# Performance work log

Hardware: AMD Instinct MI355X
Metric: run time of the kernel (lower is better)

## Reference

```python
import jax, jax.numpy as jnp
import numpy as np
from jax import lax

B, T, E, H, ENC, NUM_LAYERS = 256, 100, 300, 512, 1024, 3
FORGET_BIAS = 1.0  # BasicLSTMCell default


def lstm_scan(x, W, b):
    """BasicLSTMCell over time. x: [B,T,E], W: [E+H,4H], b: [4H] -> hs: [B,T,H]."""
    def step(carry, xt):
        c, h = carry
        z = jnp.concatenate([xt, h], axis=-1) @ W + b  # [B,4H]
        i, j, f, o = jnp.split(z, 4, axis=-1)  # TF gate order i, j, f, o
        c = c * jax.nn.sigmoid(f + FORGET_BIAS) + jax.nn.sigmoid(i) * jnp.tanh(j)
        h = jnp.tanh(c) * jax.nn.sigmoid(o)
        return (c, h), h
    init = (jnp.zeros((x.shape[0], W.shape[1] // 4), x.dtype),) * 2
    _, hs = lax.scan(step, init, jnp.swapaxes(x, 0, 1))  # scan over T
    return jnp.swapaxes(hs, 0, 1)  # [B,T,H]


def last_output(hs, lengths):
    # reverse_sequence + slice[:, 0, :] == output at step length-1
    return hs[jnp.arange(hs.shape[0]), lengths - 1]  # [B,H]


def setup_inputs() -> dict:
    key = jax.random.key(0)
    ks = jax.random.split(key, 10)
    scale = 0.01  # random_normal_initializer(stddev=1/100)
    return {
        "left_embed": jax.random.normal(ks[0], (B, T, E), jnp.float32),
        "left_lengths": jax.random.randint(ks[1], (B,), 1, T + 1, jnp.int32),
        "right_embed": jax.random.normal(ks[2], (B, T, E), jnp.float32),
        "right_lengths": jax.random.randint(ks[3], (B,), 1, T + 1, jnp.int32),
        "W_left": jax.random.normal(ks[4], (E + H, 4 * H), jnp.float32) / np.sqrt(E + H),
        "b_left": jnp.zeros((4 * H,), jnp.float32),
        "W_right": jax.random.normal(ks[5], (E + H, 4 * H), jnp.float32) / np.sqrt(E + H),
        "b_right": jnp.zeros((4 * H,), jnp.float32),
        "trans_weights": scale * jax.random.normal(ks[6], (2 * H, ENC), jnp.float32),
        "hidden_weights": scale * jax.random.normal(ks[7], (NUM_LAYERS - 1, ENC, ENC), jnp.float32),
    }


def reference(left_embed, left_lengths, right_embed, right_lengths,
              W_left, b_left, W_right, b_right, trans_weights, hidden_weights):
    l_last = last_output(lstm_scan(left_embed, W_left, b_left), left_lengths)
    r_last = last_output(lstm_scan(right_embed, W_right, b_right), right_lengths)
    ctx = jnp.concatenate([l_last, r_last], axis=1)  # [B, 2H]
    x = jax.nn.relu(ctx @ trans_weights)
    for i in range(hidden_weights.shape[0]):  # dropout keep_prob=1.0 -> identity
        x = jax.nn.relu(x @ hidden_weights[i])
    return x  # [B, ENC]
```

## Files before the change

### kernel.cpp

```cpp
#include <hip/hip_runtime.h>
#include <math.h>

#define EDIM 300
#define HDIM 512
#define TDIM 100
#define BDIM 256
#define ENC  1024
#define NBLK 256

#define B_C     0u
#define B_HPK   1048576u
#define B_WXF   3145728u
#define B_WHF   5767168u
#define B_CTX   9961472u
#define B_X1    11010048u
#define B_X2    12058624u
#define B_TWH   13107200u
#define B_TWL   19398656u
#define B_ZX    25690112u

typedef __attribute__((ext_vector_type(8))) short bf16x8;
typedef _Float16 f16x8 __attribute__((ext_vector_type(8)));
typedef __attribute__((ext_vector_type(4))) float f32x4;
typedef __attribute__((ext_vector_type(4))) unsigned int u32x4;

__device__ __forceinline__ float fast_sigmoid(float x) {
    return 1.0f / (1.0f + __expf(-x));
}
__device__ __forceinline__ float fast_tanh(float x) {
    float t = __expf(2.0f * x);
    return 1.0f - 2.0f / (t + 1.0f);
}
__device__ __forceinline__ unsigned short bf16_rne(float v) {
    unsigned int u = __float_as_uint(v);
    unsigned int r = (u + 0x7fffu + ((u >> 16) & 1u)) >> 16;
    return (unsigned short)r;
}
__device__ __forceinline__ float bf16_to_f(unsigned short h) {
    return __uint_as_float(((unsigned int)h) << 16);
}
__device__ __forceinline__ void split2(float v, unsigned short& hi, unsigned short& lo) {
    hi = bf16_rne(v);
    lo = bf16_rne(v - bf16_to_f(hi));
}
__device__ __forceinline__ unsigned short f16_bits(float v) {
    _Float16 h = (_Float16)v;
    return *(unsigned short*)&h;
}
__device__ __forceinline__ float f16_val(unsigned short u) {
    _Float16 h = *(_Float16*)&u;
    return (float)h;
}
__device__ __forceinline__ void split_f16(float v, unsigned short& hi, unsigned short& lo) {
    hi = f16_bits(v);
    lo = f16_bits(v - f16_val(hi));
}

__global__ void zero_kernel(float* __restrict__ p, int n) {
    int i = blockIdx.x * blockDim.x + threadIdx.x;
    if (i < n) p[i] = 0.0f;
}

__global__ __launch_bounds__(256) void prep_wx(
    const float* __restrict__ WL, const float* __restrict__ WR, char* __restrict__ ws)
{
    __shared__ float tile[64 * 65];
    int bid = blockIdx.x;
    int d = bid / (5 * 32);
    int rem = bid - d * (5 * 32);
    int kt = rem >> 5;
    int ct = rem & 31;
    const int k0 = kt * 64;
    const float* W = d ? WR : WL;
    for (int pass = 0; pass < 16; ++pass) {
        int idx = pass * 256 + threadIdx.x;
        int kk = idx >> 6, c = idx & 63;
        int g = (c >> 4) & 3, hl = c & 15;
        int col = g * HDIM + ct * 16 + hl;
        int kg = k0 + kk;
        tile[kk * 65 + c] = (kg < EDIM) ? W[(size_t)kg * 2048 + col] : 0.0f;
    }
    __syncthreads();
    unsigned short* wx = (unsigned short*)(ws + B_WXF) + (size_t)d * 2048 * 320;
    for (int pass = 0; pass < 16; ++pass) {
        int idx = pass * 256 + threadIdx.x;
        int c = idx >> 6, kk = idx & 63;
        wx[(size_t)(ct * 64 + c) * 320 + k0 + kk] = f16_bits(tile[kk * 65 + c]);
    }
}

__global__ __launch_bounds__(256) void prep_whf(
    const float* __restrict__ WL, const float* __restrict__ WR, char* __restrict__ ws)
{
    __shared__ float tile[64 * 65];
    int bid = blockIdx.x;
    int d = bid >> 8;
    int rem = bid & 255;
    int kt = rem >> 5;
    int ct = rem & 31;
    const float* W = d ? WR : WL;
    for (int pass = 0; pass < 16; ++pass) {
        int idx = pass * 256 + threadIdx.x;
        int kk = idx >> 6, c = idx & 63;
        int g = (c >> 4) & 3, hl = c & 15;
        int col = g * HDIM + ct * 16 + hl;
        tile[kk * 65 + c] = W[(size_t)(300 + kt * 64 + kk) * 2048 + col];
    }
    __syncthreads();
    unsigned short* dst = (unsigned short*)(ws + B_WHF) + ((size_t)(d * 32 + ct) * 64) * 512;
    #pragma unroll
    for (int p = 0; p < 2; ++p) {
        int item = p * 256 + threadIdx.x;
        int fl = item >> 6;
        int ls = item & 63;
        int itl = fl >> 2, nfl = fl & 3;
        int frag = (kt >> 2) * 32 + ((kt & 3) * 2 + itl) * 4 + nfl;
        __align__(16) unsigned short v[8];
        #pragma unroll
        for (int j = 0; j < 8; ++j)
            v[j] = f16_bits(tile[(itl * 32 + (ls >> 4) * 8 + j) * 65 + nfl * 16 + (ls & 15)]);
        *(uint4*)(dst + (size_t)frag * 512 + ls * 8) = *(uint4*)v;
    }
}

__global__ __launch_bounds__(256) void prep_w_tail(
    const float* __restrict__ TW, const float* __restrict__ HW, char* __restrict__ ws)
{
    __shared__ float tile[64 * 65];
    int bid = blockIdx.x;
    int l = bid / 256;
    int rem = bid - l * 256;
    int kt = rem >> 4, ct = rem & 15;
    const int k0 = kt * 64, n0 = ct * 64;
    const float* W = (l == 0) ? TW : (HW + (size_t)(l - 1) * ENC * ENC);
    for (int pass = 0; pass < 16; ++pass) {
        int idx = pass * 256 + threadIdx.x;
        int kk = idx >> 6, c = idx & 63;
        tile[kk * 65 + c] = W[(size_t)(k0 + kk) * ENC + n0 + c];
    }
    __syncthreads();
    unsigned short* wh = (unsigned short*)(ws + B_TWH) + (size_t)l * ENC * ENC;
    unsigned short* wl = (unsigned short*)(ws + B_TWL) + (size_t)l * ENC * ENC;
    for (int pass = 0; pass < 16; ++pass) {
        int idx = pass * 256 + threadIdx.x;
        int c = idx >> 6, kk = idx & 63;
        unsigned short hi, lo;
        split2(tile[kk * 65 + c], hi, lo);
        size_t o = (size_t)(n0 + c) * ENC + k0 + kk;
        wh[o] = hi;
        wl[o] = lo;
    }
}

__global__ __launch_bounds__(512, 4) void prep_zx(
    const float* __restrict__ xL, const float* __restrict__ xR,
    const float* __restrict__ bL, const float* __restrict__ bR,
    char* __restrict__ ws)
{
    __shared__ __align__(16) char smem[81920];
    const int ntile = blockIdx.x;
    const int m0    = blockIdx.y * 64;
    const int d     = blockIdx.z;
    const int n0    = ntile * 128;
    const float* __restrict__ x    = d ? xR : xL;
    const float* __restrict__ bias = d ? bR : bL;
    const unsigned short* __restrict__ Wxp = (const unsigned short*)(ws + B_WXF) + (size_t)d * 2048 * 320;
    unsigned short* __restrict__ zxd = (unsigned short*)(ws + B_ZX) + (size_t)d * TDIM * BDIM * 2048;

    const int tid = threadIdx.x;
    const int l   = tid & 63;
    const int w   = tid >> 6;
    const int kh  = w >> 2;
    const int ms  = w & 3;
    const int fr  = l & 15;
    const int fg  = l >> 4;

    #pragma unroll
    for (int j = 0; j < 10; ++j) {
        int c = j * 512 + tid;
        int frag = c >> 6, ls = c & 63;
        int khf = (frag >= 40) ? 1 : 0;
        int f2 = frag - khf * 40;
        int itf = f2 >> 3, nff = f2 & 7;
        int colp = n0 + nff * 16 + (ls & 15);
        int kk = khf * 160 + itf * 32 + (ls >> 4) * 8;
        *(uint4*)(smem + frag * 1024 + ls * 16) =
            *(const uint4*)(Wxp + (size_t)colp * 320 + kk);
    }
    __syncthreads();

    f32x4 acc[8] = {};
    const int rowX = m0 + ms * 16 + fr;
    const float* __restrict__ xrow = x + (size_t)rowX * EDIM;
    const int kb = kh * 160 + fg * 8;

    #pragma unroll
    for (int it = 0; it < 5; ++it) {
        const int kg = kb + it * 32;
        float4 f4a = (kg + 4 <= EDIM) ? *(const float4*)(xrow + kg) : make_float4(0.f, 0.f, 0.f, 0.f);
        float4 f4b = (kg + 8 <= EDIM) ? *(const float4*)(xrow + kg + 4) : make_float4(0.f, 0.f, 0.f, 0.f);
        __align__(16) unsigned short ahu[8], alu[8];
        float vv[8] = { f4a.x, f4a.y, f4a.z, f4a.w, f4b.x, f4b.y, f4b.z, f4b.w };
        #pragma unroll
        for (int i = 0; i < 8; ++i) {
            unsigned short hi, lo;
            split_f16(vv[i], hi, lo);
            ahu[i] = hi;
            alu[i] = lo;
        }
        const f16x8 ah = *(f16x8*)ahu;
        const f16x8 al = *(f16x8*)alu;
        #pragma unroll
        for (int nf = 0; nf < 8; ++nf) {
            const f16x8 bv = *(const f16x8*)(smem + ((kh * 40 + it * 8 + nf) << 10) + l * 16);
            acc[nf] = __builtin_amdgcn_mfma_f32_16x16x32_f16(ah, bv, acc[nf], 0, 0, 0);
            acc[nf] = __builtin_amdgcn_mfma_f32_16x16x32_f16(al, bv, acc[nf], 0, 0, 0);
        }
    }

    __syncthreads();
    float* red = (float*)smem;
    unsigned short* outT = (unsigned short*)(smem + 49152);
    if (kh == 1) {
        #pragma unroll
        for (int nf = 0; nf < 8; ++nf)
            #pragma unroll
            for (int r = 0; r < 4; ++r)
                red[(ms * 16 + fg * 4 + r) * 132 + nf * 16 + fr] = acc[nf][r];
    }
    __syncthreads();
    if (kh == 0) {
        #pragma unroll
        for (int nf = 0; nf < 8; ++nf) {
            const int col = (nf & 3) * HDIM + (ntile * 2 + (nf >> 2)) * 16 + fr;
            const float bv = bias[col];
            #pragma unroll
            for (int r = 0; r < 4; ++r) {
                float v = acc[nf][r] + red[(ms * 16 + fg * 4 + r) * 132 + nf * 16 + fr] + bv;
                outT[(ms * 16 + fg * 4 + r) * 128 + nf * 16 + fr] = f16_bits(v);
            }
        }
    }
    __syncthreads();
    {
        int row = tid >> 3, seg = tid & 7;
        int rm = m0 + row;
        int b = rm / 100;
        int tt = rm - b * 100;
        unsigned short* dstrow = zxd + ((size_t)(tt * 256 + b)) * 2048 + n0 + seg * 16;
        const unsigned short* s = outT + row * 128 + seg * 16;
        __builtin_nontemporal_store(*(const u32x4*)(s),     (u32x4*)(dstrow));
        __builtin_nontemporal_store(*(const u32x4*)(s + 8), (u32x4*)(dstrow + 8));
    }
}

__global__ __launch_bounds__(512, 1) void lstm_step_h(
    const int* __restrict__ lenL, const int* __restrict__ lenR,
    char* __restrict__ ws, int t, int par)
{
    __shared__ __align__(16) char smem[65536];

    const int bid   = blockIdx.x;
    const int ntile = (bid & 7) * 4 + ((bid >> 3) & 3);
    const int mt    = bid >> 5;
    const int n0    = ntile * 64;
    const int d     = mt >> 2;
    const int brow  = (mt & 3) * 64;

    const int* __restrict__ len = d ? lenR : lenL;

    float* __restrict__ cbuf = (float*)(ws + B_C);
    const unsigned short* __restrict__ hpk_prev = (const unsigned short*)(ws + B_HPK) + (size_t)par * 524288;
    unsigned short* __restrict__ hpk_next = (unsigned short*)(ws + B_HPK) + (size_t)(par ^ 1) * 524288;
    const unsigned short* __restrict__ WhF = (const unsigned short*)(ws + B_WHF);
    const unsigned short* __restrict__ zxd = (const unsigned short*)(ws + B_ZX) + (size_t)d * TDIM * BDIM * 2048;
    float* __restrict__ ctx = (float*)(ws + B_CTX);

    const int tid = threadIdx.x;
    const int l   = tid & 63;
    const int w   = tid >> 6;
    const int kh  = w >> 2;
    const int ms  = w & 3;
    const int fr  = l & 15;
    const int fg  = l >> 4;

    {
        const unsigned short* __restrict__ wsrc = WhF + ((size_t)(d * 32 + ntile) * 64) * 512;
        #pragma unroll
        for (int j = 0; j < 8; ++j) {
            const unsigned short* g = wsrc + (size_t)(j * 512 + tid) * 8;
            char* ldst = smem + ((size_t)(j * 512 + (w << 6)) * 16);
            __builtin_amdgcn_global_load_lds(
                (const __attribute__((address_space(1))) void*)(const void*)g,
                (__attribute__((address_space(3))) void*)(void*)ldst, 16, 0, 0);
        }
    }

    const int arow = d * BDIM + brow + ms * 16 + fr;
    const unsigned short* __restrict__ abase = hpk_prev + (size_t)arow * 1024;
    uint4 aph[8], apl[8];
    #pragma unroll
    for (int it = 0; it < 8; ++it) {
        const int kb = kh * 32 + it * 4 + fg;
        aph[it] = *(const uint4*)(abase + kb * 16);
        apl[it] = *(const uint4*)(abase + kb * 16 + 8);
    }

    const int hcol = ntile * 16 + fr;
    const int row0 = brow + ms * 16 + fg * 4;
    const int4 len4 = *(const int4*)(len + row0);
    float c_arr[4];
    unsigned short zraw[16];
    if (kh == 0) {
        const size_t cb = (size_t)(d * BDIM + row0) * HDIM + hcol;
        c_arr[0] = cbuf[cb];
        c_arr[1] = cbuf[cb + HDIM];
        c_arr[2] = cbuf[cb + 2 * HDIM];
        c_arr[3] = cbuf[cb + 3 * HDIM];
        const unsigned short* zb = zxd + ((size_t)(t * 256 + row0)) * 2048 + n0 + fr;
        #pragma unroll
        for (int r = 0; r < 4; ++r)
            #pragma unroll
            for (int nf = 0; nf < 4; ++nf)
                zraw[r * 4 + nf] = zb[r * 2048 + nf * 16];
    }
    __syncthreads();

    f32x4 acc[4] = {};
    #pragma unroll
    for (int it = 0; it < 8; ++it) {
        const f16x8 ah = *(const f16x8*)&aph[it];
        const f16x8 al = *(const f16x8*)&apl[it];
        #pragma unroll
        for (int nf = 0; nf < 4; ++nf) {
            const f16x8 bv = *(const f16x8*)(smem + ((kh * 32 + it * 4 + nf) << 10) + l * 16);
            acc[nf] = __builtin_amdgcn_mfma_f32_16x16x32_f16(ah, bv, acc[nf], 0, 0, 0);
            acc[nf] = __builtin_amdgcn_mfma_f32_16x16x32_f16(al, bv, acc[nf], 0, 0, 0);
        }
    }

    __syncthreads();
    float* red = (float*)smem;
    if (kh == 1) {
        #pragma unroll
        for (int nf = 0; nf < 4; ++nf)
            #pragma unroll
            for (int r = 0; r < 4; ++r)
                red[(ms * 16 + fg * 4 + r) * 65 + nf * 16 + fr] = acc[nf][r];
    }
    __syncthreads();
    if (kh == 0) {
        const int lens[4] = { len4.x, len4.y, len4.z, len4.w };
        #pragma unroll
        for (int r = 0; r < 4; ++r) {
            const int row = row0 + r;
            const int rb = (ms * 16 + fg * 4 + r) * 65;
            const float iv = acc[0][r] + red[rb + 0 * 16 + fr] + f16_val(zraw[r * 4 + 0]);
            const float jv = acc[1][r] + red[rb + 1 * 16 + fr] + f16_val(zraw[r * 4 + 1]);
            const float fv = acc[2][r] + red[rb + 2 * 16 + fr] + f16_val(zraw[r * 4 + 2]);
            const float ov = acc[3][r] + red[rb + 3 * 16 + fr] + f16_val(zraw[r * 4 + 3]);
            const float c_new = c_arr[r] * fast_sigmoid(fv + 1.0f)
                              + fast_sigmoid(iv) * fast_tanh(jv);
            const float h_new = fast_tanh(c_new) * fast_sigmoid(ov);
            const size_t cidx = (size_t)(d * BDIM + row) * HDIM + hcol;
            cbuf[cidx] = c_new;
            unsigned short hh, hl2;
            split_f16(h_new, hh, hl2);
            const size_t hidx = (size_t)(d * BDIM + row) * 1024 + (hcol >> 3) * 16 + (hcol & 7);
            hpk_next[hidx] = hh;
            hpk_next[hidx + 8] = hl2;
            if (t == lens[r] - 1) {
                ctx[(size_t)row * (2 * HDIM) + d * HDIM + hcol] = h_new;
            }
        }
    }
}

#define TL_AS_HI(hf) ((hf) * 5120)
#define TL_AS_LO(hf) (10240 + (hf) * 5120)
#define TL_BS_HI(hf) (20480 + (hf) * 5120)
#define TL_BS_LO(hf) (30720 + (hf) * 5120)

__global__ __launch_bounds__(512, 2) void gemm_relu_mfma(
    const float* __restrict__ A, const unsigned short* __restrict__ Wh,
    const unsigned short* __restrict__ Wl, float* __restrict__ C)
{
    const int ntile = blockIdx.x & 15;
    const int mt    = blockIdx.x >> 4;
    const int n0    = ntile * 64;
    const int m0    = mt * 64;

    __shared__ __align__(16) char smem[40960];

    const int tid  = threadIdx.x;
    const int l    = tid & 63;
    const int w    = tid >> 6;
    const int kh   = w >> 2;
    const int ms   = w & 3;
    const int fr   = l & 15;
    const int fg   = l >> 4;
    const int arow = tid >> 3;
    const int q    = (tid & 7) * 4;

    f32x4 acc[4] = {};

    for (int it = 0; it < 16; ++it) {
        #pragma unroll
        for (int hf = 0; hf < 2; ++hf) {
            const int kg = hf * 512 + it * 32 + q;
            const float4 v = *(const float4*)(A + (size_t)(m0 + arow) * ENC + kg);
            ushort4 vh, vl;
            split2(v.x, vh.x, vl.x);
            split2(v.y, vh.y, vl.y);
            split2(v.z, vh.z, vl.z);
            split2(v.w, vh.w, vl.w);
            *(ushort4*)(smem + TL_AS_HI(hf) + (arow * 40 + q) * 2) = vh;
            *(ushort4*)(smem + TL_AS_LO(hf) + (arow * 40 + q) * 2) = vl;
            const size_t wo = (size_t)(n0 + arow) * ENC + kg;
            *(ushort4*)(smem + TL_BS_HI(hf) + (arow * 40 + q) * 2) = *(const ushort4*)(Wh + wo);
            *(ushort4*)(smem + TL_BS_LO(hf) + (arow * 40 + q) * 2) = *(const ushort4*)(Wl + wo);
        }
        __syncthreads();
        const int aoff = ((ms * 16 + fr) * 40 + fg * 8) * 2;
        const bf16x8 ah = *(const bf16x8*)(smem + TL_AS_HI(kh) + aoff);
        const bf16x8 al = *(const bf16x8*)(smem + TL_AS_LO(kh) + aoff);
        #pragma unroll
        for (int nf = 0; nf < 4; ++nf) {
            const int boff = ((nf * 16 + fr) * 40 + fg * 8) * 2;
            const bf16x8 bh = *(const bf16x8*)(smem + TL_BS_HI(kh) + boff);
            const bf16x8 bl = *(const bf16x8*)(smem + TL_BS_LO(kh) + boff);
            acc[nf] = __builtin_amdgcn_mfma_f32_16x16x32_bf16(ah, bh, acc[nf], 0, 0, 0);
            acc[nf] = __builtin_amdgcn_mfma_f32_16x16x32_bf16(ah, bl, acc[nf], 0, 0, 0);
            acc[nf] = __builtin_amdgcn_mfma_f32_16x16x32_bf16(al, bh, acc[nf], 0, 0, 0);
        }
        __syncthreads();
    }

    float* red = (float*)smem;
    if (kh == 1) {
        #pragma unroll
        for (int nf = 0; nf < 4; ++nf)
            #pragma unroll
            for (int r = 0; r < 4; ++r)
                red[(ms * 16 + fg * 4 + r) * 65 + nf * 16 + fr] = acc[nf][r];
    }
    __syncthreads();
    if (kh == 0) {
        #pragma unroll
        for (int nf = 0; nf < 4; ++nf) {
            #pragma unroll
            for (int r = 0; r < 4; ++r) {
                float v = acc[nf][r] + red[(ms * 16 + fg * 4 + r) * 65 + nf * 16 + fr];
                v = v > 0.f ? v : 0.f;
                const int row = m0 + ms * 16 + fg * 4 + r;
                C[(size_t)row * ENC + n0 + nf * 16 + fr] = v;
            }
        }
    }
}

extern "C" void kernel_launch(void* const* d_in, const int* in_sizes, int n_in,
                              void* d_out, int out_size, void* d_ws, size_t ws_size,
                              hipStream_t stream) {
    const float* xL   = (const float*)d_in[0];
    const int*   lenL = (const int*)  d_in[1];
    const float* xR   = (const float*)d_in[2];
    const int*   lenR = (const int*)  d_in[3];
    const float* WL   = (const float*)d_in[4];
    const float* bL   = (const float*)d_in[5];
    const float* WR   = (const float*)d_in[6];
    const float* bR   = (const float*)d_in[7];
    const float* TW   = (const float*)d_in[8];
    const float* HW   = (const float*)d_in[9];
    char* ws   = (char*)d_ws;
    float* out = (float*)d_out;

    zero_kernel<<<3072, 256, 0, stream>>>((float*)ws, 786432);
    prep_wx<<<320, 256, 0, stream>>>(WL, WR, ws);
    prep_whf<<<512, 256, 0, stream>>>(WL, WR, ws);
    prep_w_tail<<<768, 256, 0, stream>>>(TW, HW, ws);
    prep_zx<<<dim3(16, 400, 2), 512, 0, stream>>>(xL, xR, bL, bR, ws);

    for (int t = 0; t < TDIM; ++t) {
        lstm_step_h<<<NBLK, 512, 0, stream>>>(lenL, lenR, ws, t, t & 1);
    }

    float* ctx = (float*)(ws + B_CTX);
    float* x1  = (float*)(ws + B_X1);
    float* x2  = (float*)(ws + B_X2);
    const unsigned short* twh = (const unsigned short*)(ws + B_TWH);
    const unsigned short* twl = (const unsigned short*)(ws + B_TWL);
    gemm_relu_mfma<<<64, 512, 0, stream>>>(ctx, twh,                twl,                x1);
    gemm_relu_mfma<<<64, 512, 0, stream>>>(x1,  twh + 1024 * 1024, twl + 1024 * 1024,  x2);
    gemm_relu_mfma<<<64, 512, 0, stream>>>(x2,  twh + 2048 * 1024, twl + 2048 * 1024,  out);
}
```

Measured before the change: 1.306 ms.

## Make prep_zx persistent over row tiles and split warps by N instead of K

The input-projection kernel now launches 16 row groups instead of 400, and each block loops over 25 row tiles of 64 rows. The staged weight tile is therefore loaded into shared memory once and reused across many tiles. Warps now partition the output columns rather than the K dimension, which removes the cross-warp shared-memory reduction and the extra barriers. The trade-off is that results are written straight to global memory as scattered 2-byte stores instead of coalesced 16-byte nontemporal stores, and the grid has far fewer blocks.

```diff
diff --git a/kernel.cpp b/kernel.cpp
--- a/kernel.cpp
+++ b/kernel.cpp
@@ -22,7 +22,6 @@
 typedef __attribute__((ext_vector_type(8))) short bf16x8;
 typedef _Float16 f16x8 __attribute__((ext_vector_type(8)));
 typedef __attribute__((ext_vector_type(4))) float f32x4;
-typedef __attribute__((ext_vector_type(4))) unsigned int u32x4;
 
 __device__ __forceinline__ float fast_sigmoid(float x) {
     return 1.0f / (1.0f + __expf(-x));
@@ -159,7 +158,7 @@
 {
     __shared__ __align__(16) char smem[81920];
     const int ntile = blockIdx.x;
-    const int m0    = blockIdx.y * 64;
+    const int mg    = blockIdx.y;
     const int d     = blockIdx.z;
     const int n0    = ntile * 128;
     const float* __restrict__ x    = d ? xR : xL;
@@ -170,7 +169,7 @@
     const int tid = threadIdx.x;
     const int l   = tid & 63;
     const int w   = tid >> 6;
-    const int kh  = w >> 2;
+    const int nh  = w >> 2;
     const int ms  = w & 3;
     const int fr  = l & 15;
     const int fg  = l >> 4;
@@ -179,78 +178,58 @@
     for (int j = 0; j < 10; ++j) {
         int c = j * 512 + tid;
         int frag = c >> 6, ls = c & 63;
-        int khf = (frag >= 40) ? 1 : 0;
-        int f2 = frag - khf * 40;
-        int itf = f2 >> 3, nff = f2 & 7;
-        int colp = n0 + nff * 16 + (ls & 15);
-        int kk = khf * 160 + itf * 32 + (ls >> 4) * 8;
+        int nfg = frag / 10, itf = frag - nfg * 10;
+        int colp = n0 + nfg * 16 + (ls & 15);
+        int kk = itf * 32 + (ls >> 4) * 8;
         *(uint4*)(smem + frag * 1024 + ls * 16) =
             *(const uint4*)(Wxp + (size_t)colp * 320 + kk);
     }
     __syncthreads();
 
-    f32x4 acc[8] = {};
-    const int rowX = m0 + ms * 16 + fr;
-    const float* __restrict__ xrow = x + (size_t)rowX * EDIM;
-    const int kb = kh * 160 + fg * 8;
-
-    #pragma unroll
-    for (int it = 0; it < 5; ++it) {
-        const int kg = kb + it * 32;
-        float4 f4a = (kg + 4 <= EDIM) ? *(const float4*)(xrow + kg) : make_float4(0.f, 0.f, 0.f, 0.f);
-        float4 f4b = (kg + 8 <= EDIM) ? *(const float4*)(xrow + kg + 4) : make_float4(0.f, 0.f, 0.f, 0.f);
-        __align__(16) unsigned short ahu[8], alu[8];
-        float vv[8] = { f4a.x, f4a.y, f4a.z, f4a.w, f4b.x, f4b.y, f4b.z, f4b.w };
-        #pragma unroll
-        for (int i = 0; i < 8; ++i) {
-            unsigned short hi, lo;
-            split_f16(vv[i], hi, lo);
-            ahu[i] = hi;
-            alu[i] = lo;
-        }
-        const f16x8 ah = *(f16x8*)ahu;
-        const f16x8 al = *(f16x8*)alu;
-        #pragma unroll
-        for (int nf = 0; nf < 8; ++nf) {
-            const f16x8 bv = *(const f16x8*)(smem + ((kh * 40 + it * 8 + nf) << 10) + l * 16);
-            acc[nf] = __builtin_amdgcn_mfma_f32_16x16x32_f16(ah, bv, acc[nf], 0, 0, 0);
-            acc[nf] = __builtin_amdgcn_mfma_f32_16x16x32_f16(al, bv, acc[nf], 0, 0, 0);
-        }
-    }
-
-    __syncthreads();
-    float* red = (float*)smem;
-    unsigned short* outT = (unsigned short*)(smem + 49152);
-    if (kh == 1) {
-        #pragma unroll
-        for (int nf = 0; nf < 8; ++nf)
-            #pragma unroll
-            for (int r = 0; r < 4; ++r)
-                red[(ms * 16 + fg * 4 + r) * 132 + nf * 16 + fr] = acc[nf][r];
-    }
-    __syncthreads();
-    if (kh == 0) {
-        #pragma unroll
-        for (int nf = 0; nf < 8; ++nf) {
-            const int col = (nf & 3) * HDIM + (ntile * 2 + (nf >> 2)) * 16 + fr;
-            const float bv = bias[col];
+    for (int mi = 0; mi < 25; ++mi) {
+        const int m0 = (mg * 25 + mi) * 64;
+        const int rowX = m0 + ms * 16 + fr;
+        const float* __restrict__ xrow = x + (size_t)rowX * EDIM;
+
+        f32x4 acc[4] = {};
+        #pragma unroll
+        for (int it = 0; it < 10; ++it) {
+            const int kg = it * 32 + fg * 8;
+            float4 f4a = (kg + 4 <= EDIM) ? *(const float4*)(xrow + kg) : make_float4(0.f, 0.f, 0.f, 0.f);
+            float4 f4b = (kg + 8 <= EDIM) ? *(const float4*)(xrow + kg + 4) : make_float4(0.f, 0.f, 0.f, 0.f);
+            __align__(16) unsigned short ahu[8], alu[8];
+            float vv[8] = { f4a.x, f4a.y, f4a.z, f4a.w, f4b.x, f4b.y, f4b.z, f4b.w };
+            #pragma unroll
+            for (int i = 0; i < 8; ++i) {
+                unsigned short hi, lo;
+                split_f16(vv[i], hi, lo);
+                ahu[i] = hi;
+                alu[i] = lo;
+            }
+            const f16x8 ah = *(f16x8*)ahu;
+            const f16x8 al = *(f16x8*)alu;
+            #pragma unroll
+            for (int nf = 0; nf < 4; ++nf) {
+                const int frag = (nh * 4 + nf) * 10 + it;
+                const f16x8 bv = *(const f16x8*)(smem + (frag << 10) + l * 16);
+                acc[nf] = __builtin_amdgcn_mfma_f32_16x16x32_f16(ah, bv, acc[nf], 0, 0, 0);
+                acc[nf] = __builtin_amdgcn_mfma_f32_16x16x32_f16(al, bv, acc[nf], 0, 0, 0);
+            }
+        }
+
+        #pragma unroll
+        for (int nf = 0; nf < 4; ++nf) {
+            const int colp = n0 + nh * 64 + nf * 16 + fr;
+            const int G = colp >> 6, g = (colp >> 4) & 3, hl = colp & 15;
+            const float bv = bias[g * HDIM + G * 16 + hl];
             #pragma unroll
             for (int r = 0; r < 4; ++r) {
-                float v = acc[nf][r] + red[(ms * 16 + fg * 4 + r) * 132 + nf * 16 + fr] + bv;
-                outT[(ms * 16 + fg * 4 + r) * 128 + nf * 16 + fr] = f16_bits(v);
+                const int rm = m0 + ms * 16 + fg * 4 + r;
+                const int b = rm / 100;
+                const int tt = rm - b * 100;
+                zxd[((size_t)(tt * 256 + b)) * 2048 + colp] = f16_bits(acc[nf][r] + bv);
             }
         }
-    }
-    __syncthreads();
-    {
-        int row = tid >> 3, seg = tid & 7;
-        int rm = m0 + row;
-        int b = rm / 100;
-        int tt = rm - b * 100;
-        unsigned short* dstrow = zxd + ((size_t)(tt * 256 + b)) * 2048 + n0 + seg * 16;
-        const unsigned short* s = outT + row * 128 + seg * 16;
-        __builtin_nontemporal_store(*(const u32x4*)(s),     (u32x4*)(dstrow));
-        __builtin_nontemporal_store(*(const u32x4*)(s + 8), (u32x4*)(dstrow + 8));
     }
 }
 
@@ -479,7 +458,7 @@
     prep_wx<<<320, 256, 0, stream>>>(WL, WR, ws);
     prep_whf<<<512, 256, 0, stream>>>(WL, WR, ws);
     prep_w_tail<<<768, 256, 0, stream>>>(TW, HW, ws);
-    prep_zx<<<dim3(16, 400, 2), 512, 0, stream>>>(xL, xR, bL, bR, ws);
+    prep_zx<<<dim3(16, 16, 2), 512, 0, stream>>>(xL, xR, bL, bR, ws);
 
     for (int t = 0; t < TDIM; ++t) {
         lstm_step_h<<<NBLK, 512, 0, stream>>>(lenL, lenR, ws, t, t & 1);
```

Measured after the change: 1.553 ms. 18.9% more time.

## Pre-swizzle Wx into MFMA fragment slabs and stream them to LDS asynchronously

Applied to the files above, without the earlier changes.

prep_wxf now writes the input-projection weights already laid out as per-tile MFMA B-fragments, so each prep_zx block can copy a contiguous slab straight into LDS with global_load_lds instead of gathering strided rows through registers. The x-row loads are hoisted ahead of the barrier so they overlap with the async LDS fill. The zx output stores also switch from nontemporal to regular stores. This trades a more complex prep layout for cheaper, coalesced weight staging in the large zx GEMM; the plain stores may change cache behaviour on the large zx buffer.

```diff
diff --git a/kernel.cpp b/kernel.cpp
--- a/kernel.cpp
+++ b/kernel.cpp
@@ -22,7 +22,6 @@
 typedef __attribute__((ext_vector_type(8))) short bf16x8;
 typedef _Float16 f16x8 __attribute__((ext_vector_type(8)));
 typedef __attribute__((ext_vector_type(4))) float f32x4;
-typedef __attribute__((ext_vector_type(4))) unsigned int u32x4;
 
 __device__ __forceinline__ float fast_sigmoid(float x) {
     return 1.0f / (1.0f + __expf(-x));
@@ -61,31 +60,39 @@
     if (i < n) p[i] = 0.0f;
 }
 
-__global__ __launch_bounds__(256) void prep_wx(
+__global__ __launch_bounds__(256) void prep_wxf(
     const float* __restrict__ WL, const float* __restrict__ WR, char* __restrict__ ws)
 {
-    __shared__ float tile[64 * 65];
+    __shared__ float tile[32 * 130];
     int bid = blockIdx.x;
-    int d = bid / (5 * 32);
-    int rem = bid - d * (5 * 32);
-    int kt = rem >> 5;
-    int ct = rem & 31;
-    const int k0 = kt * 64;
+    int d = bid / 160;
+    int rem = bid - d * 160;
+    int ktt = rem >> 4;
+    int nt  = rem & 15;
+    const int kh  = ktt / 5;
+    const int itt = ktt - kh * 5;
+    const int k0  = kh * 160 + itt * 32;
     const float* W = d ? WR : WL;
     for (int pass = 0; pass < 16; ++pass) {
         int idx = pass * 256 + threadIdx.x;
-        int kk = idx >> 6, c = idx & 63;
-        int g = (c >> 4) & 3, hl = c & 15;
-        int col = g * HDIM + ct * 16 + hl;
+        int kk = idx >> 7, c = idx & 127;
+        int colp = nt * 128 + c;
+        int G = colp >> 6, g = (colp >> 4) & 3, hl = colp & 15;
+        int col = g * HDIM + G * 16 + hl;
         int kg = k0 + kk;
-        tile[kk * 65 + c] = (kg < EDIM) ? W[(size_t)kg * 2048 + col] : 0.0f;
-    }
-    __syncthreads();
-    unsigned short* wx = (unsigned short*)(ws + B_WXF) + (size_t)d * 2048 * 320;
-    for (int pass = 0; pass < 16; ++pass) {
-        int idx = pass * 256 + threadIdx.x;
-        int c = idx >> 6, kk = idx & 63;
-        wx[(size_t)(ct * 64 + c) * 320 + k0 + kk] = f16_bits(tile[kk * 65 + c]);
+        tile[kk * 130 + c] = (kg < EDIM) ? W[(size_t)kg * 2048 + col] : 0.0f;
+    }
+    __syncthreads();
+    unsigned short* slab = (unsigned short*)(ws + B_WXF) + (size_t)(d * 16 + nt) * 80 * 512;
+    #pragma unroll
+    for (int p = 0; p < 2; ++p) {
+        int item = p * 256 + threadIdx.x;
+        int nf = item >> 6, ls = item & 63;
+        __align__(16) unsigned short v[8];
+        #pragma unroll
+        for (int j = 0; j < 8; ++j)
+            v[j] = f16_bits(tile[((ls >> 4) * 8 + j) * 130 + nf * 16 + (ls & 15)]);
+        *(uint4*)(slab + (size_t)(kh * 40 + itt * 8 + nf) * 512 + ls * 8) = *(uint4*)v;
     }
 }
 
@@ -161,10 +168,9 @@
     const int ntile = blockIdx.x;
     const int m0    = blockIdx.y * 64;
     const int d     = blockIdx.z;
-    const int n0    = ntile * 128;
     const float* __restrict__ x    = d ? xR : xL;
     const float* __restrict__ bias = d ? bR : bL;
-    const unsigned short* __restrict__ Wxp = (const unsigned short*)(ws + B_WXF) + (size_t)d * 2048 * 320;
+    const unsigned short* __restrict__ WxF = (const unsigned short*)(ws + B_WXF);
     unsigned short* __restrict__ zxd = (unsigned short*)(ws + B_ZX) + (size_t)d * TDIM * BDIM * 2048;
 
     const int tid = threadIdx.x;
@@ -175,32 +181,36 @@
     const int fr  = l & 15;
     const int fg  = l >> 4;
 
-    #pragma unroll
-    for (int j = 0; j < 10; ++j) {
-        int c = j * 512 + tid;
-        int frag = c >> 6, ls = c & 63;
-        int khf = (frag >= 40) ? 1 : 0;
-        int f2 = frag - khf * 40;
-        int itf = f2 >> 3, nff = f2 & 7;
-        int colp = n0 + nff * 16 + (ls & 15);
-        int kk = khf * 160 + itf * 32 + (ls >> 4) * 8;
-        *(uint4*)(smem + frag * 1024 + ls * 16) =
-            *(const uint4*)(Wxp + (size_t)colp * 320 + kk);
-    }
-    __syncthreads();
-
-    f32x4 acc[8] = {};
+    {
+        const unsigned short* __restrict__ wsrc = WxF + (size_t)(d * 16 + ntile) * 80 * 512;
+        #pragma unroll
+        for (int j = 0; j < 10; ++j) {
+            const unsigned short* g = wsrc + (size_t)(j * 512 + tid) * 8;
+            char* ldst = smem + ((size_t)(j * 512 + (w << 6)) * 16);
+            __builtin_amdgcn_global_load_lds(
+                (const __attribute__((address_space(1))) void*)(const void*)g,
+                (__attribute__((address_space(3))) void*)(void*)ldst, 16, 0, 0);
+        }
+    }
+
     const int rowX = m0 + ms * 16 + fr;
     const float* __restrict__ xrow = x + (size_t)rowX * EDIM;
     const int kb = kh * 160 + fg * 8;
-
+    float4 xa[5], xb[5];
     #pragma unroll
     for (int it = 0; it < 5; ++it) {
         const int kg = kb + it * 32;
-        float4 f4a = (kg + 4 <= EDIM) ? *(const float4*)(xrow + kg) : make_float4(0.f, 0.f, 0.f, 0.f);
-        float4 f4b = (kg + 8 <= EDIM) ? *(const float4*)(xrow + kg + 4) : make_float4(0.f, 0.f, 0.f, 0.f);
+        xa[it] = (kg + 4 <= EDIM) ? *(const float4*)(xrow + kg)     : make_float4(0.f, 0.f, 0.f, 0.f);
+        xb[it] = (kg + 8 <= EDIM) ? *(const float4*)(xrow + kg + 4) : make_float4(0.f, 0.f, 0.f, 0.f);
+    }
+    __syncthreads();
+
+    f32x4 acc[8] = {};
+    #pragma unroll
+    for (int it = 0; it < 5; ++it) {
         __align__(16) unsigned short ahu[8], alu[8];
-        float vv[8] = { f4a.x, f4a.y, f4a.z, f4a.w, f4b.x, f4b.y, f4b.z, f4b.w };
+        float vv[8] = { xa[it].x, xa[it].y, xa[it].z, xa[it].w,
+                        xb[it].x, xb[it].y, xb[it].z, xb[it].w };
         #pragma unroll
         for (int i = 0; i < 8; ++i) {
             unsigned short hi, lo;
@@ -247,10 +257,10 @@
         int rm = m0 + row;
         int b = rm / 100;
         int tt = rm - b * 100;
-        unsigned short* dstrow = zxd + ((size_t)(tt * 256 + b)) * 2048 + n0 + seg * 16;
+        unsigned short* dstrow = zxd + ((size_t)(tt * 256 + b)) * 2048 + ntile * 128 + seg * 16;
         const unsigned short* s = outT + row * 128 + seg * 16;
-        __builtin_nontemporal_store(*(const u32x4*)(s),     (u32x4*)(dstrow));
-        __builtin_nontemporal_store(*(const u32x4*)(s + 8), (u32x4*)(dstrow + 8));
+        *(uint4*)(dstrow)     = *(const uint4*)(s);
+        *(uint4*)(dstrow + 8) = *(const uint4*)(s + 8);
     }
 }
 
@@ -476,7 +486,7 @@
     float* out = (float*)d_out;
 
     zero_kernel<<<3072, 256, 0, stream>>>((float*)ws, 786432);
-    prep_wx<<<320, 256, 0, stream>>>(WL, WR, ws);
+    prep_wxf<<<320, 256, 0, stream>>>(WL, WR, ws);
     prep_whf<<<512, 256, 0, stream>>>(WL, WR, ws);
     prep_w_tail<<<768, 256, 0, stream>>>(TW, HW, ws);
     prep_zx<<<dim3(16, 400, 2), 512, 0, stream>>>(xL, xR, bL, bR, ws);
```

After: 1.296 ms. Within noise of the previous version (-0.7%).
